# Kernel optimization log

Hardware: AMD Instinct MI355X
Metric: run time of the kernel (lower is better)

The kernel has to match this reference:

```python
import jax, jax.numpy as jnp
import numpy as np

NUM_USERS = 100000
NUM_ITEMS = 50000
D = 64
NUM_LAYERS = 2
NNZ_H = 3200000
NNZ_I = 3000000
EPS = 1e-12


def setup_inputs() -> dict:
    key = jax.random.key(0)
    ks = jax.random.split(key, 24)
    inp = {}
    inp['user_emb'] = jax.random.normal(ks[0], (NUM_USERS, D), jnp.float32) * 0.1
    inp['item_emb'] = jax.random.normal(ks[1], (NUM_ITEMS, D), jnp.float32) * 0.1
    inp['gating_w'] = jax.random.normal(ks[2], (4, D, D), jnp.float32) * 0.1
    inp['gating_b'] = jax.random.normal(ks[3], (4, 1, D), jnp.float32) * 0.1
    inp['sgating_w'] = jax.random.normal(ks[4], (3, D, D), jnp.float32) * 0.1
    inp['sgating_b'] = jax.random.normal(ks[5], (3, 1, D), jnp.float32) * 0.1
    inp['att_mat'] = jax.random.normal(ks[6], (D, D), jnp.float32) * 0.1
    inp['att_agg'] = jax.random.normal(ks[7], (1, D), jnp.float32) * 0.1
    inp['hs_row'] = jax.random.randint(ks[8], (NNZ_H,), 0, NUM_USERS, jnp.int32)
    inp['hs_col'] = jax.random.randint(ks[9], (NNZ_H,), 0, NUM_USERS, jnp.int32)
    inp['hs_val'] = jax.random.uniform(ks[10], (NNZ_H,), jnp.float32) / 32.0
    inp['hj_row'] = jax.random.randint(ks[11], (NNZ_H,), 0, NUM_USERS, jnp.int32)
    inp['hj_col'] = jax.random.randint(ks[12], (NNZ_H,), 0, NUM_USERS, jnp.int32)
    inp['hj_val'] = jax.random.uniform(ks[13], (NNZ_H,), jnp.float32) / 32.0
    inp['hp_row'] = jax.random.randint(ks[14], (NNZ_H,), 0, NUM_USERS, jnp.int32)
    inp['hp_col'] = jax.random.randint(ks[15], (NNZ_H,), 0, NUM_USERS, jnp.int32)
    inp['hp_val'] = jax.random.uniform(ks[16], (NNZ_H,), jnp.float32) / 32.0
    inp['inter_row'] = jax.random.randint(ks[17], (NNZ_I,), 0, NUM_USERS, jnp.int32)
    inp['inter_col'] = jax.random.randint(ks[18], (NNZ_I,), 0, NUM_ITEMS, jnp.int32)
    inp['inter_val'] = jax.random.uniform(ks[19], (NNZ_I,), jnp.float32) / 32.0
    return inp


def spmm(row, col, val, x, n_rows):
    # sparse (n_rows x m) @ dense (m x d), COO edges
    return jax.ops.segment_sum(val[:, None] * x[col], row, num_segments=n_rows)


def l2norm(x):
    return x / jnp.maximum(jnp.linalg.norm(x, axis=1, keepdims=True), EPS)


def self_gating(em, w, b):
    return em * jax.nn.sigmoid(em @ w + b)


def channel_attention(embs, att_mat, att_agg):
    # embs: list of 3 arrays [N, D]
    w = jnp.stack([jnp.sum(att_agg * (e @ att_mat), axis=1) for e in embs])  # [3, N]
    score = jax.nn.softmax(w, axis=0)
    mixed = score[0][:, None] * embs[0] + score[1][:, None] * embs[1] + score[2][:, None] * embs[2]
    return mixed, score


def reference(user_emb, item_emb, gating_w, gating_b, sgating_w, sgating_b,
              att_mat, att_agg,
              hs_row, hs_col, hs_val, hj_row, hj_col, hj_val,
              hp_row, hp_col, hp_val, inter_row, inter_col, inter_val):
    u_c0 = self_gating(user_emb, gating_w[0], gating_b[0])
    u_c1 = self_gating(user_emb, gating_w[1], gating_b[1])
    u_c2 = self_gating(user_emb, gating_w[2], gating_b[2])
    u_simple = self_gating(user_emb, gating_w[3], gating_b[3])
    it = item_emb
    acc_c0, acc_c1, acc_c2 = u_c0, u_c1, u_c2
    acc_simple, acc_item = u_simple, it
    for _ in range(NUM_LAYERS):
        mixed, _ = channel_attention([u_c0, u_c1, u_c2], att_mat, att_agg)
        mixed = (mixed + u_simple) / 2.0
        u_c0 = spmm(hs_row, hs_col, hs_val, u_c0, NUM_USERS)
        acc_c0 = acc_c0 + l2norm(u_c0)
        u_c1 = spmm(hj_row, hj_col, hj_val, u_c1, NUM_USERS)
        acc_c1 = acc_c1 + l2norm(u_c1)
        u_c2 = spmm(hp_row, hp_col, hp_val, u_c2, NUM_USERS)
        acc_c2 = acc_c2 + l2norm(u_c2)
        new_item = spmm(inter_col, inter_row, inter_val, mixed, NUM_ITEMS)  # inter^T @ mixed
        acc_item = acc_item + l2norm(new_item)
        u_simple = spmm(inter_row, inter_col, inter_val, it, NUM_USERS)  # inter @ item (old)
        acc_simple = acc_simple + l2norm(u_simple)
        it = new_item
    final_user, _ = channel_attention([acc_c0, acc_c1, acc_c2], att_mat, att_agg)
    final_user = final_user + acc_simple / 2.0
    sg0 = self_gating(final_user, sgating_w[0], sgating_b[0])
    sg1 = self_gating(final_user, sgating_w[1], sgating_b[1])
    sg2 = self_gating(final_user, sgating_w[2], sgating_b[2])
    return final_user, acc_item, sg0, sg1, sg2
```

## Files before the change

kernel.cpp:

```cpp
#include <hip/hip_runtime.h>

#define D 64
#define EPS 1e-12f

#define SB 6
#define BSZ (1 << SB)
#define NBMAX 2048
#define NCHUNK 128

__device__ __forceinline__ float wave_sum(float v) {
#pragma unroll
  for (int off = 32; off > 0; off >>= 1) v += __shfl_xor(v, off, 64);
  return v;
}

__global__ void compute_v_kernel(const float* __restrict__ att_mat,
                                 const float* __restrict__ att_agg,
                                 float* __restrict__ v) {
  int d = threadIdx.x;
  float s = 0.f;
#pragma unroll
  for (int j = 0; j < D; ++j) s += att_mat[d * D + j] * att_agg[j];
  v[d] = s;
}

__global__ __launch_bounds__(256) void gating4_kernel(
    const float* __restrict__ emb, const float* __restrict__ W,
    const float* __restrict__ B, float* __restrict__ u0, float* __restrict__ u1,
    float* __restrict__ u2, float* __restrict__ u3, float* __restrict__ a0,
    float* __restrict__ a1, float* __restrict__ a2, float* __restrict__ a3,
    int nrows) {
  __shared__ float4 sW4[D * D];
  for (int i = threadIdx.x; i < D * D; i += blockDim.x)
    sW4[i] = make_float4(W[i], W[D * D + i], W[2 * D * D + i],
                         W[3 * D * D + i]);
  __syncthreads();
  int lane = threadIdx.x & 63;
  int wid = (blockIdx.x * blockDim.x + threadIdx.x) >> 6;
  int nw = (gridDim.x * blockDim.x) >> 6;
  float b0 = B[0 * D + lane], b1 = B[1 * D + lane];
  float b2 = B[2 * D + lane], b3 = B[3 * D + lane];
  for (int r0 = wid * 4; r0 < nrows; r0 += nw * 4) {
    float e[4];
    float y[4][4];
#pragma unroll
    for (int i = 0; i < 4; ++i) {
      int r = r0 + i < nrows ? r0 + i : r0;
      e[i] = emb[(size_t)r * D + lane];
      y[i][0] = b0; y[i][1] = b1; y[i][2] = b2; y[i][3] = b3;
    }
#pragma unroll 16
    for (int j = 0; j < D; ++j) {
      float4 w = sW4[j * D + lane];
#pragma unroll
      for (int i = 0; i < 4; ++i) {
        float ej = __shfl(e[i], j, 64);
        y[i][0] += ej * w.x;
        y[i][1] += ej * w.y;
        y[i][2] += ej * w.z;
        y[i][3] += ej * w.w;
      }
    }
#pragma unroll
    for (int i = 0; i < 4; ++i) {
      int r = r0 + i;
      if (r < nrows) {
        size_t idx = (size_t)r * D + lane;
        float o0 = e[i] / (1.f + __expf(-y[i][0]));
        float o1 = e[i] / (1.f + __expf(-y[i][1]));
        float o2 = e[i] / (1.f + __expf(-y[i][2]));
        float o3 = e[i] / (1.f + __expf(-y[i][3]));
        u0[idx] = o0; u1[idx] = o1; u2[idx] = o2; u3[idx] = o3;
        if (a0) { a0[idx] = o0; a1[idx] = o1; a2[idx] = o2; a3[idx] = o3; }
      }
    }
  }
}

__global__ __launch_bounds__(256) void sgating3_kernel(
    const float* __restrict__ x, const float* __restrict__ W,
    const float* __restrict__ B, float* __restrict__ o0f,
    float* __restrict__ o1f, float* __restrict__ o2f, int nrows) {
  __shared__ float4 sW4[D * D];
  for (int i = threadIdx.x; i < D * D; i += blockDim.x)
    sW4[i] = make_float4(W[i], W[D * D + i], W[2 * D * D + i], 0.f);
  __syncthreads();
  int lane = threadIdx.x & 63;
  int wid = (blockIdx.x * blockDim.x + threadIdx.x) >> 6;
  int nw = (gridDim.x * blockDim.x) >> 6;
  float b0 = B[0 * D + lane], b1 = B[1 * D + lane], b2 = B[2 * D + lane];
  for (int r0 = wid * 4; r0 < nrows; r0 += nw * 4) {
    float e[4];
    float y[4][3];
#pragma unroll
    for (int i = 0; i < 4; ++i) {
      int r = r0 + i < nrows ? r0 + i : r0;
      e[i] = x[(size_t)r * D + lane];
      y[i][0] = b0; y[i][1] = b1; y[i][2] = b2;
    }
#pragma unroll 16
    for (int j = 0; j < D; ++j) {
      float4 w = sW4[j * D + lane];
#pragma unroll
      for (int i = 0; i < 4; ++i) {
        float ej = __shfl(e[i], j, 64);
        y[i][0] += ej * w.x;
        y[i][1] += ej * w.y;
        y[i][2] += ej * w.z;
      }
    }
#pragma unroll
    for (int i = 0; i < 4; ++i) {
      int r = r0 + i;
      if (r < nrows) {
        size_t idx = (size_t)r * D + lane;
        o0f[idx] = e[i] / (1.f + __expf(-y[i][0]));
        o1f[idx] = e[i] / (1.f + __expf(-y[i][1]));
        o2f[idx] = e[i] / (1.f + __expf(-y[i][2]));
      }
    }
  }
}

__global__ __launch_bounds__(256) void attn_mix_kernel(
    const float* __restrict__ u0, const float* __restrict__ u1,
    const float* __restrict__ u2, const float* __restrict__ us,
    const float* __restrict__ v, float* __restrict__ mixed, int nrows) {
  int lane = threadIdx.x & 63;
  int wid = (blockIdx.x * blockDim.x + threadIdx.x) >> 6;
  if (wid >= nrows) return;
  int idx = wid * D + lane;
  float e0 = u0[idx], e1 = u1[idx], e2 = u2[idx], eu = us[idx];
  float vd = v[lane];
  float w0 = wave_sum(e0 * vd);
  float w1 = wave_sum(e1 * vd);
  float w2 = wave_sum(e2 * vd);
  float m = fmaxf(w0, fmaxf(w1, w2));
  float s0 = __expf(w0 - m), s1 = __expf(w1 - m), s2 = __expf(w2 - m);
  float inv = 1.f / (s0 + s1 + s2);
  mixed[idx] = ((s0 * e0 + s1 * e1 + s2 * e2) * inv + eu) * 0.5f;
}

__global__ __launch_bounds__(256) void final_attn_kernel(
    const float* __restrict__ a0, const float* __restrict__ a1,
    const float* __restrict__ a2, const float* __restrict__ as,
    const float* __restrict__ v, float* __restrict__ out, int nrows) {
  int lane = threadIdx.x & 63;
  int wid = (blockIdx.x * blockDim.x + threadIdx.x) >> 6;
  if (wid >= nrows) return;
  int idx = wid * D + lane;
  float e0 = a0[idx], e1 = a1[idx], e2 = a2[idx], eu = as[idx];
  float vd = v[lane];
  float w0 = wave_sum(e0 * vd);
  float w1 = wave_sum(e1 * vd);
  float w2 = wave_sum(e2 * vd);
  float m = fmaxf(w0, fmaxf(w1, w2));
  float s0 = __expf(w0 - m), s1 = __expf(w1 - m), s2 = __expf(w2 - m);
  float inv = 1.f / (s0 + s1 + s2);
  out[idx] = (s0 * e0 + s1 * e1 + s2 * e2) * inv + 0.5f * eu;
}

__global__ __launch_bounds__(256) void l2acc_kernel(const float* __restrict__ x,
                                                    float* __restrict__ acc,
                                                    int nrows) {
  int lane = threadIdx.x & 63;
  int wid = (blockIdx.x * blockDim.x + threadIdx.x) >> 6;
  if (wid >= nrows) return;
  int idx = wid * D + lane;
  float xv = x[idx];
  float ss = wave_sum(xv * xv);
  float nrm = fmaxf(sqrtf(ss), EPS);
  acc[idx] += xv / nrm;
}

__global__ __launch_bounds__(256) void spmm_atomic_kernel(
    const int* __restrict__ row, const int* __restrict__ col,
    const float* __restrict__ val, const float* __restrict__ x,
    float* __restrict__ out, int nnz) {
  int lane = threadIdx.x & 63;
  int wid = (blockIdx.x * blockDim.x + threadIdx.x) >> 6;
  int nw = (gridDim.x * blockDim.x) >> 6;
  for (int base = wid * 64; base < nnz; base += nw * 64) {
    int e = base + lane;
    int r = 0, c = 0;
    float v = 0.f;
    if (e < nnz) { r = row[e]; c = col[e]; v = val[e]; }
    int cnt = nnz - base; if (cnt > 64) cnt = 64;
    for (int i = 0; i < cnt; ++i) {
      int ri = __shfl(r, i, 64);
      int ci = __shfl(c, i, 64);
      float vi = __shfl(v, i, 64);
      float xv = x[ci * D + lane];
      atomicAdd(&out[ri * D + lane], vi * xv);
    }
  }
}


__global__ __launch_bounds__(256) void hist_kernel(const int* __restrict__ row,
                                                   int* __restrict__ counts,
                                                   int nnz) {
  int i = blockIdx.x * blockDim.x + threadIdx.x;
  int n = gridDim.x * blockDim.x;
  for (; i < nnz; i += n) atomicAdd(&counts[row[i]], 1);
}

__global__ __launch_bounds__(256) void scan1_kernel(const int* __restrict__ in,
                                                    int* __restrict__ out,
                                                    int* __restrict__ partials,
                                                    int n) {
  __shared__ int lds[256];
  int t = threadIdx.x;
  int base = blockIdx.x * 2048 + t * 8;
  int v[8];
  int s = 0;
#pragma unroll
  for (int k = 0; k < 8; ++k) {
    int i = base + k;
    v[k] = (i < n) ? in[i] : 0;
    s += v[k];
  }
  lds[t] = s;
  __syncthreads();
  for (int ofs = 1; ofs < 256; ofs <<= 1) {
    int add = 0;
    if (t >= ofs) add = lds[t - ofs];
    __syncthreads();
    if (t >= ofs) lds[t] += add;
    __syncthreads();
  }
  int excl = lds[t] - s;
  if (t == 255) partials[blockIdx.x] = lds[255];
  int run = excl;
#pragma unroll
  for (int k = 0; k < 8; ++k) {
    int i = base + k;
    if (i < n) out[i] = run;
    run += v[k];
  }
}

__global__ __launch_bounds__(256) void scan2_kernel(int* __restrict__ partials,
                                                    int P) {
  __shared__ int lds[256];
  int t = threadIdx.x;
  int s = (t < P) ? partials[t] : 0;
  lds[t] = s;
  __syncthreads();
  for (int ofs = 1; ofs < 256; ofs <<= 1) {
    int add = 0;
    if (t >= ofs) add = lds[t - ofs];
    __syncthreads();
    if (t >= ofs) lds[t] += add;
    __syncthreads();
  }
  if (t < P) partials[t] = lds[t] - s;
}

__global__ __launch_bounds__(256) void scan3_kernel(
    int* __restrict__ out, const int* __restrict__ partials, int n) {
  int i = blockIdx.x * blockDim.x + threadIdx.x;
  int nt = gridDim.x * blockDim.x;
  for (; i < n; i += nt) out[i] += partials[i >> 11];
}

__global__ __launch_bounds__(256) void bhist_kernel(
    const int* __restrict__ row, int* __restrict__ bh, int nnz, int nb,
    int chunk) {
  __shared__ int hist[NBMAX];
  for (int i = threadIdx.x; i < nb; i += blockDim.x) hist[i] = 0;
  __syncthreads();
  int base = blockIdx.x * chunk;
  int lim = base + chunk;
  if (lim > nnz) lim = nnz;
  for (int e = base + threadIdx.x; e < lim; e += blockDim.x)
    atomicAdd(&hist[row[e] >> SB], 1);
  __syncthreads();
  int* o = bh + (size_t)blockIdx.x * nb;
  for (int i = threadIdx.x; i < nb; i += blockDim.x) o[i] = hist[i];
}

__global__ __launch_bounds__(256) void chunkscan_kernel(
    const int* __restrict__ bh, int* __restrict__ fo, int nnz, int nb,
    int chunk) {
  __shared__ int lds[256];
  int k = blockIdx.x;
  int base = k * chunk;
  int t = threadIdx.x;
  const int* in = bh + (size_t)k * nb;
  int v[8];
  int s = 0;
#pragma unroll
  for (int q = 0; q < 8; ++q) {
    int b = t * 8 + q;
    v[q] = (b < nb) ? in[b] : 0;
    s += v[q];
  }
  lds[t] = s;
  __syncthreads();
  for (int ofs = 1; ofs < 256; ofs <<= 1) {
    int add = 0;
    if (t >= ofs) add = lds[t - ofs];
    __syncthreads();
    if (t >= ofs) lds[t] += add;
    __syncthreads();
  }
  int run = base + lds[t] - s;
  int* o = fo + (size_t)k * (nb + 1);
#pragma unroll
  for (int q = 0; q < 8; ++q) {
    int b = t * 8 + q;
    if (b < nb) o[b] = run;
    run += v[q];
  }
  if (t == 255) o[nb] = run;
}

__global__ __launch_bounds__(256) void bscatter2_kernel(
    const int* __restrict__ row, const int* __restrict__ col,
    const float* __restrict__ val, const int* __restrict__ fo,
    int2* __restrict__ staging, int nnz, int nb, int chunk) {
  __shared__ int cur[NBMAX];
  const int* o = fo + (size_t)blockIdx.x * (nb + 1);
  for (int i = threadIdx.x; i < nb; i += blockDim.x) cur[i] = o[i];
  __syncthreads();
  int base = blockIdx.x * chunk;
  int lim = base + chunk;
  if (lim > nnz) lim = nnz;
  for (int e = base + threadIdx.x; e < lim; e += blockDim.x) {
    int r = row[e];
    int b = r >> SB;
    int idx = atomicAdd(&cur[b], 1);
    staging[idx] =
        make_int2(((r & (BSZ - 1)) << 24) | col[e], __float_as_int(val[e]));
  }
}

__global__ __launch_bounds__(256) void bucket_gather_kernel(
    const int* __restrict__ row_ptr, const int* __restrict__ fo,
    const int2* __restrict__ staging, int2* __restrict__ edges_out, int nrows,
    int nb) {
  __shared__ int lfill[BSZ];
  __shared__ int2 sfrag[NCHUNK];
  int b = blockIdx.x;
  int t = threadIdx.x;
  if (t < BSZ) {
    int r = (b << SB) + t;
    lfill[t] = row_ptr[r < nrows ? r : nrows];
  }
  if (t < NCHUNK) {
    const int* o = fo + (size_t)t * (nb + 1) + b;
    sfrag[t] = make_int2(o[0], o[1]);
  }
  __syncthreads();
  int lane = t & 63;
  int w = t >> 6;
  for (int k = w; k < NCHUNK; k += 4) {
    int2 f = sfrag[k];
    for (int e = f.x + lane; e < f.y; e += 64) {
      int2 ev = staging[e];
      int lrow = ((unsigned)ev.x) >> 24;
      int idx = atomicAdd(&lfill[lrow], 1);
      edges_out[idx] = make_int2(ev.x & 0xFFFFFF, ev.y);
    }
  }
}

__global__ __launch_bounds__(256) void spmm_csr_l2acc_kernel(
    const int* __restrict__ row_ptr, const int2* __restrict__ edges,
    const float* __restrict__ x, float* __restrict__ out,
    float* __restrict__ acc, const float* __restrict__ init, int nrows) {
  int lane = threadIdx.x & 63;
  int r = (blockIdx.x * blockDim.x + threadIdx.x) >> 6;
  if (r >= nrows) return;
  int start = row_ptr[r], end = row_ptr[r + 1];
  float sum = 0.f;
  for (int j = start; j < end; j += 64) {
    int e = j + lane;
    int c = 0;
    float v = 0.f;
    if (e < end) {
      int2 ev = edges[e];
      c = ev.x;
      v = __int_as_float(ev.y);
    }
    int cnt = end - j;
    if (cnt > 64) cnt = 64;
    int i = 0;
    for (; i + 4 <= cnt; i += 4) {
      int c0 = __shfl(c, i, 64);
      int c1 = __shfl(c, i + 1, 64);
      int c2 = __shfl(c, i + 2, 64);
      int c3 = __shfl(c, i + 3, 64);
      float v0 = __shfl(v, i, 64);
      float v1 = __shfl(v, i + 1, 64);
      float v2 = __shfl(v, i + 2, 64);
      float v3 = __shfl(v, i + 3, 64);
      float x0 = x[c0 * D + lane];
      float x1 = x[c1 * D + lane];
      float x2 = x[c2 * D + lane];
      float x3 = x[c3 * D + lane];
      sum += v0 * x0;
      sum += v1 * x1;
      sum += v2 * x2;
      sum += v3 * x3;
    }
    for (; i < cnt; ++i) {
      int ci = __shfl(c, i, 64);
      float vi = __shfl(v, i, 64);
      sum += vi * x[ci * D + lane];
    }
  }
  int idx = r * D + lane;
  out[idx] = sum;
  float ss = wave_sum(sum * sum);
  float nrm = fmaxf(sqrtf(ss), EPS);
  float base = init ? init[idx] : acc[idx];
  acc[idx] = base + sum / nrm;
}


static void build_csr(const int* row, const int* col, const float* val, int nnz,
                      int nrows, int* counts, int* row_ptr, int* partials,
                      int* bh, int* fo, int2* staging, int2* edges_out,
                      hipStream_t stream) {
  int n1 = nrows + 1;
  hipMemsetAsync(counts, 0, n1 * sizeof(int), stream);
  hipLaunchKernelGGL(hist_kernel, dim3(1024), dim3(256), 0, stream, row, counts,
                     nnz);
  int nblk = (n1 + 2047) / 2048;
  hipLaunchKernelGGL(scan1_kernel, dim3(nblk), dim3(256), 0, stream, counts,
                     row_ptr, partials, n1);
  hipLaunchKernelGGL(scan2_kernel, dim3(1), dim3(256), 0, stream, partials,
                     nblk);
  hipLaunchKernelGGL(scan3_kernel, dim3(64), dim3(256), 0, stream, row_ptr,
                     partials, n1);
  int nb = (nrows + BSZ - 1) >> SB;
  int chunk = (nnz + NCHUNK - 1) / NCHUNK;
  hipLaunchKernelGGL(bhist_kernel, dim3(NCHUNK), dim3(256), 0, stream, row, bh,
                     nnz, nb, chunk);
  hipLaunchKernelGGL(chunkscan_kernel, dim3(NCHUNK), dim3(256), 0, stream, bh,
                     fo, nnz, nb, chunk);
  hipLaunchKernelGGL(bscatter2_kernel, dim3(NCHUNK), dim3(256), 0, stream, row,
                     col, val, fo, staging, nnz, nb, chunk);
  hipLaunchKernelGGL(bucket_gather_kernel, dim3(nb), dim3(256), 0, stream,
                     row_ptr, fo, staging, edges_out, nrows, nb);
}

extern "C" void kernel_launch(void* const* d_in, const int* in_sizes, int n_in,
                              void* d_out, int out_size, void* d_ws,
                              size_t ws_size, hipStream_t stream) {
  const float* user_emb = (const float*)d_in[0];
  const float* item_emb = (const float*)d_in[1];
  const float* gating_w = (const float*)d_in[2];
  const float* gating_b = (const float*)d_in[3];
  const float* sgating_w = (const float*)d_in[4];
  const float* sgating_b = (const float*)d_in[5];
  const float* att_mat = (const float*)d_in[6];
  const float* att_agg = (const float*)d_in[7];
  const int* hs_row = (const int*)d_in[8];
  const int* hs_col = (const int*)d_in[9];
  const float* hs_val = (const float*)d_in[10];
  const int* hj_row = (const int*)d_in[11];
  const int* hj_col = (const int*)d_in[12];
  const float* hj_val = (const float*)d_in[13];
  const int* hp_row = (const int*)d_in[14];
  const int* hp_col = (const int*)d_in[15];
  const float* hp_val = (const float*)d_in[16];
  const int* inter_row = (const int*)d_in[17];
  const int* inter_col = (const int*)d_in[18];
  const float* inter_val = (const float*)d_in[19];

  const int U = in_sizes[0] / D;
  const int I = in_sizes[1] / D;
  const int NH = in_sizes[8];
  const int NI = in_sizes[17];
  const size_t UD = (size_t)U * D;
  const size_t ID = (size_t)I * D;

  float* out = (float*)d_out;
  float* final_user = out;
  float* acc_item = out + UD;
  float* sg0 = out + UD + ID;
  float* sg1 = sg0 + UD;
  float* sg2 = sg1 + UD;
  float* acc0 = sg0, *acc1 = sg1, *acc2 = sg2, *accS = final_user;

  char* p = (char*)d_ws;
  auto alloc = [&](size_t bytes) -> void* {
    void* r = (void*)p;
    p += (bytes + 255) & ~(size_t)255;
    return r;
  };
  float* u0 = (float*)alloc(UD * 4);
  float* u1 = (float*)alloc(UD * 4);
  float* u2 = (float*)alloc(UD * 4);
  float* us = (float*)alloc(UD * 4);
  float* mixed = (float*)alloc(UD * 4);
  float* spare = (float*)alloc(UD * 4);
  float* it_a = (float*)alloc(ID * 4);
  float* it_b = (float*)alloc(ID * 4);
  float* v = (float*)alloc(256 * 4);
  int* partials = (int*)alloc(256 * 4);
  int* cnt_u = (int*)alloc((U + 2) * 4);
  int* cnt_i = (int*)alloc((I + 2) * 4);
  int* bh = (int*)alloc((size_t)NCHUNK * NBMAX * 4);
  int* fo = (int*)alloc((size_t)NCHUNK * (NBMAX + 1) * 4);
  int* rp_hs = (int*)alloc((U + 2) * 4);
  int* rp_hj = (int*)alloc((U + 2) * 4);
  int* rp_hp = (int*)alloc((U + 2) * 4);
  int* rp_iu = (int*)alloc((U + 2) * 4);
  int* rp_ii = (int*)alloc((I + 2) * 4);
  size_t NMAX = (size_t)(NH > NI ? NH : NI);
  int2* staging;
  if (NMAX * 8 <= UD * 4) staging = (int2*)spare;
  else staging = (int2*)alloc(NMAX * 8);
  int2* ed_hs = (int2*)alloc((size_t)NH * 8);
  int2* ed_hj = (int2*)alloc((size_t)NH * 8);
  int2* ed_hp = (int2*)alloc((size_t)NH * 8);
  int2* ed_iu = (int2*)alloc((size_t)NI * 8);
  int2* ed_ii = (int2*)alloc((size_t)NI * 8);
  size_t needed = (size_t)(p - (char*)d_ws);
  bool use_csr = needed <= ws_size && U < (1 << 24) && I < (1 << 24) &&
                 U <= NBMAX * BSZ && I <= NBMAX * BSZ;

  const int ROWB_U = (U + 3) / 4;
  const int ROWB_I = (I + 3) / 4;
  const int SPMM_BLOCKS = 2048;

  hipLaunchKernelGGL(compute_v_kernel, dim3(1), dim3(64), 0, stream, att_mat,
                     att_agg, v);
  hipLaunchKernelGGL(gating4_kernel, dim3(512), dim3(256), 0, stream, user_emb,
                     gating_w, gating_b, u0, u1, u2, us,
                     use_csr ? (float*)nullptr : acc0,
                     use_csr ? (float*)nullptr : acc1,
                     use_csr ? (float*)nullptr : acc2,
                     use_csr ? (float*)nullptr : accS, U);
  if (!use_csr) {
    hipMemcpyAsync(acc_item, item_emb, ID * sizeof(float),
                   hipMemcpyDeviceToDevice, stream);
    hipMemcpyAsync(it_a, item_emb, ID * sizeof(float), hipMemcpyDeviceToDevice,
                   stream);
  }

  if (use_csr) {
    build_csr(hs_row, hs_col, hs_val, NH, U, cnt_u, rp_hs, partials, bh, fo,
              staging, ed_hs, stream);
    build_csr(hj_row, hj_col, hj_val, NH, U, cnt_u, rp_hj, partials, bh, fo,
              staging, ed_hj, stream);
    build_csr(hp_row, hp_col, hp_val, NH, U, cnt_u, rp_hp, partials, bh, fo,
              staging, ed_hp, stream);
    build_csr(inter_row, inter_col, inter_val, NI, U, cnt_u, rp_iu, partials,
              bh, fo, staging, ed_iu, stream);
    build_csr(inter_col, inter_row, inter_val, NI, I, cnt_i, rp_ii, partials,
              bh, fo, staging, ed_ii, stream);
  }

  const float* it_src = item_emb;
  float* it_dst = it_b;
  float* it_old = it_a;
  float* it_new = it_b;

  for (int layer = 0; layer < 2; ++layer) {
    hipLaunchKernelGGL(attn_mix_kernel, dim3(ROWB_U), dim3(256), 0, stream, u0,
                       u1, u2, us, v, mixed, U);
    if (use_csr) {
      const float* i0 = (layer == 0) ? u0 : nullptr;
      const float* i1 = (layer == 0) ? u1 : nullptr;
      const float* i2 = (layer == 0) ? u2 : nullptr;
      const float* ii = (layer == 0) ? item_emb : nullptr;
      const float* is = (layer == 0) ? us : nullptr;
      hipLaunchKernelGGL(spmm_csr_l2acc_kernel, dim3(ROWB_U), dim3(256), 0,
                         stream, rp_hs, ed_hs, u0, spare, acc0, i0, U);
      { float* t = u0; u0 = spare; spare = t; }
      hipLaunchKernelGGL(spmm_csr_l2acc_kernel, dim3(ROWB_U), dim3(256), 0,
                         stream, rp_hj, ed_hj, u1, spare, acc1, i1, U);
      { float* t = u1; u1 = spare; spare = t; }
      hipLaunchKernelGGL(spmm_csr_l2acc_kernel, dim3(ROWB_U), dim3(256), 0,
                         stream, rp_hp, ed_hp, u2, spare, acc2, i2, U);
      { float* t = u2; u2 = spare; spare = t; }
      hipLaunchKernelGGL(spmm_csr_l2acc_kernel, dim3(ROWB_I), dim3(256), 0,
                         stream, rp_ii, ed_ii, mixed, it_dst, acc_item, ii, I);
      hipLaunchKernelGGL(spmm_csr_l2acc_kernel, dim3(ROWB_U), dim3(256), 0,
                         stream, rp_iu, ed_iu, it_src, spare, accS, is, U);
      { float* t = us; us = spare; spare = t; }
      it_src = it_dst;
      it_dst = it_a;
    } else {
      hipMemsetAsync(spare, 0, UD * sizeof(float), stream);
      hipLaunchKernelGGL(spmm_atomic_kernel, dim3(SPMM_BLOCKS), dim3(256), 0,
                         stream, hs_row, hs_col, hs_val, u0, spare, NH);
      hipLaunchKernelGGL(l2acc_kernel, dim3(ROWB_U), dim3(256), 0, stream,
                         spare, acc0, U);
      { float* t = u0; u0 = spare; spare = t; }
      hipMemsetAsync(spare, 0, UD * sizeof(float), stream);
      hipLaunchKernelGGL(spmm_atomic_kernel, dim3(SPMM_BLOCKS), dim3(256), 0,
                         stream, hj_row, hj_col, hj_val, u1, spare, NH);
      hipLaunchKernelGGL(l2acc_kernel, dim3(ROWB_U), dim3(256), 0, stream,
                         spare, acc1, U);
      { float* t = u1; u1 = spare; spare = t; }
      hipMemsetAsync(spare, 0, UD * sizeof(float), stream);
      hipLaunchKernelGGL(spmm_atomic_kernel, dim3(SPMM_BLOCKS), dim3(256), 0,
                         stream, hp_row, hp_col, hp_val, u2, spare, NH);
      hipLaunchKernelGGL(l2acc_kernel, dim3(ROWB_U), dim3(256), 0, stream,
                         spare, acc2, U);
      { float* t = u2; u2 = spare; spare = t; }
      hipMemsetAsync(it_new, 0, ID * sizeof(float), stream);
      hipLaunchKernelGGL(spmm_atomic_kernel, dim3(SPMM_BLOCKS), dim3(256), 0,
                         stream, inter_col, inter_row, inter_val, mixed, it_new,
                         NI);
      hipLaunchKernelGGL(l2acc_kernel, dim3(ROWB_I), dim3(256), 0, stream,
                         it_new, acc_item, I);
      hipMemsetAsync(spare, 0, UD * sizeof(float), stream);
      hipLaunchKernelGGL(spmm_atomic_kernel, dim3(SPMM_BLOCKS), dim3(256), 0,
                         stream, inter_row, inter_col, inter_val, it_old, spare,
                         NI);
      hipLaunchKernelGGL(l2acc_kernel, dim3(ROWB_U), dim3(256), 0, stream,
                         spare, accS, U);
      { float* t = us; us = spare; spare = t; }
      { float* t = it_old; it_old = it_new; it_new = t; }
    }
  }

  hipLaunchKernelGGL(final_attn_kernel, dim3(ROWB_U), dim3(256), 0, stream,
                     acc0, acc1, acc2, accS, v, final_user, U);
  hipLaunchKernelGGL(sgating3_kernel, dim3(512), dim3(256), 0, stream,
                     final_user, sgating_w, sgating_b, sg0, sg1, sg2, U);
}
```

Baseline: 3.216 ms.

## Locally bucket-sort chunks in LDS before coalesced scatter; raise chunk count

The COO-to-CSR build now uses 1024 chunks instead of 128. Each chunk's edges are bucketed into shared memory first and then written contiguously to staging, replacing scattered global writes with coalesced ones. The gather kernel now assigns one thread per chunk fragment and walks it serially, since fragments become small. The bucket histogram aliases the last edge buffer to save workspace. The risks are larger LDS use per block (32KB buffer plus counters), lower occupancy, more fragment bookkeeping per bucket, and serial per-thread loops in the gather.

```diff
diff --git a/kernel.cpp b/kernel.cpp
--- a/kernel.cpp
+++ b/kernel.cpp
@@ -6,7 +6,8 @@
 #define SB 6
 #define BSZ (1 << SB)
 #define NBMAX 2048
-#define NCHUNK 128
+#define NCHUNK 1024
+#define CMAX 4096
 
 __device__ __forceinline__ float wave_sum(float v) {
 #pragma unroll
@@ -316,24 +317,29 @@
   if (t == 255) o[nb] = run;
 }
 
-__global__ __launch_bounds__(256) void bscatter2_kernel(
+__global__ __launch_bounds__(256) void bsort_scatter_kernel(
     const int* __restrict__ row, const int* __restrict__ col,
     const float* __restrict__ val, const int* __restrict__ fo,
     int2* __restrict__ staging, int nnz, int nb, int chunk) {
   __shared__ int cur[NBMAX];
-  const int* o = fo + (size_t)blockIdx.x * (nb + 1);
-  for (int i = threadIdx.x; i < nb; i += blockDim.x) cur[i] = o[i];
-  __syncthreads();
-  int base = blockIdx.x * chunk;
+  __shared__ int2 sbuf[CMAX];
+  int k = blockIdx.x;
+  int base = k * chunk;
+  const int* o = fo + (size_t)k * (nb + 1);
+  for (int i = threadIdx.x; i < nb; i += blockDim.x) cur[i] = o[i] - base;
+  __syncthreads();
   int lim = base + chunk;
   if (lim > nnz) lim = nnz;
+  int cnt = lim - base;
   for (int e = base + threadIdx.x; e < lim; e += blockDim.x) {
     int r = row[e];
     int b = r >> SB;
     int idx = atomicAdd(&cur[b], 1);
-    staging[idx] =
+    sbuf[idx] =
         make_int2(((r & (BSZ - 1)) << 24) | col[e], __float_as_int(val[e]));
   }
+  __syncthreads();
+  for (int i = threadIdx.x; i < cnt; i += blockDim.x) staging[base + i] = sbuf[i];
 }
 
 __global__ __launch_bounds__(256) void bucket_gather_kernel(
@@ -348,16 +354,14 @@
     int r = (b << SB) + t;
     lfill[t] = row_ptr[r < nrows ? r : nrows];
   }
-  if (t < NCHUNK) {
-    const int* o = fo + (size_t)t * (nb + 1) + b;
-    sfrag[t] = make_int2(o[0], o[1]);
-  }
-  __syncthreads();
-  int lane = t & 63;
-  int w = t >> 6;
-  for (int k = w; k < NCHUNK; k += 4) {
+  for (int k = t; k < NCHUNK; k += blockDim.x) {
+    const int* o = fo + (size_t)k * (nb + 1) + b;
+    sfrag[k] = make_int2(o[0], o[1]);
+  }
+  __syncthreads();
+  for (int k = t; k < NCHUNK; k += blockDim.x) {
     int2 f = sfrag[k];
-    for (int e = f.x + lane; e < f.y; e += 64) {
+    for (int e = f.x; e < f.y; ++e) {
       int2 ev = staging[e];
       int lrow = ((unsigned)ev.x) >> 24;
       int idx = atomicAdd(&lfill[lrow], 1);
@@ -441,8 +445,8 @@
                      nnz, nb, chunk);
   hipLaunchKernelGGL(chunkscan_kernel, dim3(NCHUNK), dim3(256), 0, stream, bh,
                      fo, nnz, nb, chunk);
-  hipLaunchKernelGGL(bscatter2_kernel, dim3(NCHUNK), dim3(256), 0, stream, row,
-                     col, val, fo, staging, nnz, nb, chunk);
+  hipLaunchKernelGGL(bsort_scatter_kernel, dim3(NCHUNK), dim3(256), 0, stream,
+                     row, col, val, fo, staging, nnz, nb, chunk);
   hipLaunchKernelGGL(bucket_gather_kernel, dim3(nb), dim3(256), 0, stream,
                      row_ptr, fo, staging, edges_out, nrows, nb);
 }
@@ -504,8 +508,10 @@
   int* partials = (int*)alloc(256 * 4);
   int* cnt_u = (int*)alloc((U + 2) * 4);
   int* cnt_i = (int*)alloc((I + 2) * 4);
-  int* bh = (int*)alloc((size_t)NCHUNK * NBMAX * 4);
-  int* fo = (int*)alloc((size_t)NCHUNK * (NBMAX + 1) * 4);
+  const int NB_U = (U + BSZ - 1) >> SB;
+  const int NB_I = (I + BSZ - 1) >> SB;
+  const int NB_MAXU = (NB_U > NB_I ? NB_U : NB_I);
+  int* fo = (int*)alloc((size_t)NCHUNK * (NB_MAXU + 1) * 4);
   int* rp_hs = (int*)alloc((U + 2) * 4);
   int* rp_hj = (int*)alloc((U + 2) * 4);
   int* rp_hp = (int*)alloc((U + 2) * 4);
@@ -520,9 +526,12 @@
   int2* ed_hp = (int2*)alloc((size_t)NH * 8);
   int2* ed_iu = (int2*)alloc((size_t)NI * 8);
   int2* ed_ii = (int2*)alloc((size_t)NI * 8);
+  int* bh = (int*)ed_ii;
+  bool bh_fits = (size_t)NCHUNK * NB_MAXU * 4 <= (size_t)NI * 8;
   size_t needed = (size_t)(p - (char*)d_ws);
   bool use_csr = needed <= ws_size && U < (1 << 24) && I < (1 << 24) &&
-                 U <= NBMAX * BSZ && I <= NBMAX * BSZ;
+                 U <= NBMAX * BSZ && I <= NBMAX * BSZ && bh_fits &&
+                 NH <= NCHUNK * CMAX && NI <= NCHUNK * CMAX;
 
   const int ROWB_U = (U + 3) / 4;
   const int ROWB_I = (I + 3) / 4;
```

Result: faster. 2.796 ms (-13.1%).
